# Optimization experiments

Hardware: AMD Instinct MI355X
Metric: run time of the kernel (lower is better)

Reference implementation:

```python
import jax, jax.numpy as jnp
import numpy as np

N_WORDS = 30000
EMB_DIM = 784          # must be a perfect square
MAT_DIM = 28           # sqrt(784)
BATCH = 256
SEQ_LEN = 64


def setup_inputs() -> dict:
    key = jax.random.key(0)
    k_sent, k_w = jax.random.split(key)
    # token ids in [1, N_WORDS]; row 0 of the table is the identity (neutral) element
    sent = jax.random.randint(k_sent, (BATCH, SEQ_LEN), 1, N_WORDS + 1, dtype=jnp.int64) \
        if jax.config.jax_enable_x64 else \
        jax.random.randint(k_sent, (BATCH, SEQ_LEN), 1, N_WORDS + 1, dtype=jnp.int32)
    # 'identity' initialization: N(0, 0.1) + flattened identity, prepended identity neutral row
    eye_flat = jnp.eye(MAT_DIM, dtype=jnp.float32).reshape(-1)        # [784]
    init_w = 0.1 * jax.random.normal(k_w, (N_WORDS, EMB_DIM), dtype=jnp.float32) + eye_flat
    lookup_weight = jnp.concatenate([eye_flat[None, :], init_w], axis=0)  # [N_WORDS+1, 784]
    return {"sent": sent, "lookup_weight": lookup_weight}


def reference(sent, lookup_weight):
    # CMOW: embedding lookup, reshape each word vector to a 28x28 matrix,
    # then a left-to-right chain of matrix products over the sequence.
    B, S = sent.shape
    mats = lookup_weight[sent].reshape(B, S, MAT_DIM, MAT_DIM)   # [B, S, 28, 28]
    # Log-depth parallel prefix product over the sequence axis (matmul is associative).
    prods = jax.lax.associative_scan(lambda a, b: a @ b, mats, axis=1)
    cur_emb = prods[:, -1]                                       # [B, 28, 28]
    return cur_emb.reshape(-1, EMB_DIM)                          # [B, 784]
```

## Files before the change

kernel.cpp:

```cpp
#include <hip/hip_runtime.h>
#include <hip/hip_bf16.h>


typedef float f32x4  __attribute__((ext_vector_type(4)));
typedef float f32x16 __attribute__((ext_vector_type(16)));
typedef short bf16x8 __attribute__((ext_vector_type(8)));

namespace {
constexpr int MD  = 28;
constexpr int EMB = 784;
constexpr int SEQ = 64;
constexpr int BATCH = 256;
constexpr int SEG = 16;
constexpr int LEN = 4;
constexpr int RLP = 33;
}

__device__ __forceinline__ bf16x8 mkfrag(uint32_t w0, uint32_t w1,
                                         uint32_t w2, uint32_t w3) {
  union { uint32_t w[4]; bf16x8 b; } u;
  u.w[0] = w0; u.w[1] = w1; u.w[2] = w2; u.w[3] = w3;
  return u.b;
}

__device__ __forceinline__ void split8(const float* x, bf16x8& hi, bf16x8& lo) {
  uint32_t H[4], L[4];
#pragma unroll
  for (int p = 0; p < 4; ++p) {
    float x0 = x[2 * p], x1 = x[2 * p + 1];
    uint32_t h0 = __float_as_uint(x0) & 0xffff0000u;
    uint32_t h1 = __float_as_uint(x1) & 0xffff0000u;
    float l0 = x0 - __uint_as_float(h0);
    float l1 = x1 - __uint_as_float(h1);
    H[p] = (h0 >> 16) | h1;
    L[p] = (__float_as_uint(l0) >> 16) | (__float_as_uint(l1) & 0xffff0000u);
  }
  hi = mkfrag(H[0], H[1], H[2], H[3]);
  lo = mkfrag(L[0], L[1], L[2], L[3]);
}

__global__ __launch_bounds__(64)
__attribute__((amdgpu_waves_per_eu(3, 4)))
void w2m_partial_mfma(const int* __restrict__ sent,
                      const float* __restrict__ W,
                      float* __restrict__ ws) {
  __shared__ __align__(16) float Ms[1024];
  __shared__ __align__(16) float RL[32 * RLP];

  const int blk   = blockIdx.x;
  const int batch = blk >> 4;
  const int seg   = blk & 15;
  const int lane  = threadIdx.x;
  const int n = lane & 31;
  const int h = lane >> 5;
  const int* srow = sent + batch * SEQ + seg * LEN;

  if (lane < 60) *reinterpret_cast<f32x4*>(&Ms[784 + 4 * lane]) =
      (f32x4){0.f, 0.f, 0.f, 0.f};

  f32x4 st0, st1, st2, st3;
  auto gstage = [&](int t) {
    const f32x4* src = reinterpret_cast<const f32x4*>(W + (size_t)srow[t] * EMB);
    st0 = src[lane];
    st1 = src[64 + lane];
    st2 = src[128 + lane];
    if (lane < 4) st3 = src[192 + lane];
  };
  auto lpublish = [&]() {
    f32x4* d_ = reinterpret_cast<f32x4*>(Ms);
    d_[lane] = st0;
    d_[64 + lane] = st1;
    d_[128 + lane] = st2;
    if (lane < 4) d_[192 + lane] = st3;
  };

  float a[16];
  {
    const float* __restrict__ M0 = W + (size_t)srow[0] * EMB;
    const int m = n;
#pragma unroll
    for (int K = 0; K < 2; ++K)
#pragma unroll
      for (int u = 0; u < 2; ++u) {
        int k0 = 16 * K + 8 * h + 4 * u;
        f32x4 v = {0.f, 0.f, 0.f, 0.f};
        if (m < MD && k0 < MD)
          v = *reinterpret_cast<const f32x4*>(M0 + m * MD + k0);
        a[K * 8 + 4 * u + 0] = v[0];
        a[K * 8 + 4 * u + 1] = v[1];
        a[K * 8 + 4 * u + 2] = v[2];
        a[K * 8 + 4 * u + 3] = v[3];
      }
  }

  gstage(1);
  lpublish();
  gstage(2);

  f32x16 d;
#pragma unroll
  for (int t = 1; t < LEN; ++t) {
    float bb[16];
#pragma unroll
    for (int K = 0; K < 2; ++K)
#pragma unroll
      for (int e = 0; e < 8; ++e) {
        int k = 16 * K + 8 * h + e;
        bb[K * 8 + e] = Ms[k * MD + n];
      }

    bf16x8 ah0, al0, ah1, al1, bh0, bl0, bh1, bl1;
    split8(a,      ah0, al0);
    split8(a + 8,  ah1, al1);
    split8(bb,     bh0, bl0);
    split8(bb + 8, bh1, bl1);

#pragma unroll
    for (int q = 0; q < 16; ++q) d[q] = 0.f;
    d = __builtin_amdgcn_mfma_f32_32x32x16_bf16(ah0, bh0, d, 0, 0, 0);
    d = __builtin_amdgcn_mfma_f32_32x32x16_bf16(ah0, bl0, d, 0, 0, 0);
    d = __builtin_amdgcn_mfma_f32_32x32x16_bf16(al0, bh0, d, 0, 0, 0);
    d = __builtin_amdgcn_mfma_f32_32x32x16_bf16(ah1, bh1, d, 0, 0, 0);
    d = __builtin_amdgcn_mfma_f32_32x32x16_bf16(ah1, bl1, d, 0, 0, 0);
    d = __builtin_amdgcn_mfma_f32_32x32x16_bf16(al1, bh1, d, 0, 0, 0);

    if (t < LEN - 1) {
      lpublish();
      if (t + 2 < LEN) gstage(t + 2);

#pragma unroll
      for (int e = 0; e < 16; ++e) {
        int r = (e & 3) + 8 * (e >> 2) + 4 * h;
        RL[r * RLP + n] = d[e];
      }
      const int m = n;
#pragma unroll
      for (int K = 0; K < 2; ++K)
#pragma unroll
        for (int e = 0; e < 8; ++e) {
          int k = 16 * K + 8 * h + e;
          a[K * 8 + e] = RL[m * RLP + k];
        }
    }
  }

  float* pb = ws + (size_t)(batch * SEG + seg) * EMB;
  if (n < MD) {
    if ((seg & 1) == 0) {
#pragma unroll
      for (int q = 0; q < 4; ++q) {
        int rbase = 8 * q + 4 * h;
        if (rbase < MD) {
          f32x4 v = { d[4 * q], d[4 * q + 1], d[4 * q + 2], d[4 * q + 3] };
          *reinterpret_cast<f32x4*>(pb + n * MD + rbase) = v;
        }
      }
    } else {
#pragma unroll
      for (int e = 0; e < 16; ++e) {
        int r = (e & 3) + 8 * (e >> 2) + 4 * h;
        if (r < MD) pb[r * MD + n] = d[e];
      }
    }
  }
}


__device__ __forceinline__ void kloop(const float* __restrict__ A,
                                      const float* __restrict__ B,
                                      int r0, int c0,
                                      f32x4& a0, f32x4& a1, f32x4& a2, f32x4& a3) {
  f32x4 z = {0.f, 0.f, 0.f, 0.f};
  a0 = a1 = a2 = a3 = z;
#pragma unroll
  for (int k = 0; k < MD; ++k) {
    f32x4 rv = *reinterpret_cast<const f32x4*>(A + k * MD + r0);
    f32x4 mv = *reinterpret_cast<const f32x4*>(B + k * MD + c0);
    a0 += rv[0] * mv;
    a1 += rv[1] * mv;
    a2 += rv[2] * mv;
    a3 += rv[3] * mv;
  }
}

__device__ __forceinline__ void store_T(float* __restrict__ D, int r0, int c0,
                                        const f32x4& a0, const f32x4& a1,
                                        const f32x4& a2, const f32x4& a3) {
#pragma unroll
  for (int cc = 0; cc < 4; ++cc) {
    f32x4 v = { a0[cc], a1[cc], a2[cc], a3[cc] };
    *reinterpret_cast<f32x4*>(D + (c0 + cc) * MD + r0) = v;
  }
}

__device__ __forceinline__ void store_N(float* __restrict__ D, int r0, int c0,
                                        const f32x4& a0, const f32x4& a1,
                                        const f32x4& a2, const f32x4& a3) {
  *reinterpret_cast<f32x4*>(D + (r0 + 0) * MD + c0) = a0;
  *reinterpret_cast<f32x4*>(D + (r0 + 1) * MD + c0) = a1;
  *reinterpret_cast<f32x4*>(D + (r0 + 2) * MD + c0) = a2;
  *reinterpret_cast<f32x4*>(D + (r0 + 3) * MD + c0) = a3;
}

__global__ __launch_bounds__(512, 1)
void w2m_combine(const float* __restrict__ ws, float* __restrict__ out) {
  __shared__ __align__(16) float P[SEG][EMB];
  __shared__ __align__(16) float Q8[8][EMB];
  __shared__ __align__(16) float Q4[4][EMB];
  __shared__ __align__(16) float Q2[2][EMB];

  const int batch = blockIdx.x;
  const int tid   = threadIdx.x;
  const int w     = tid >> 6;
  const int lane  = tid & 63;
  const bool act  = lane < 49;
  const int i = lane / 7, j = lane % 7;
  const int r0 = 4 * i, c0 = 4 * j;

  {
    const f32x4* src = reinterpret_cast<const f32x4*>(ws + (size_t)batch * SEG * EMB);
    f32x4* dst = reinterpret_cast<f32x4*>(&P[0][0]);
    for (int u = tid; u < SEG * EMB / 4; u += 512) dst[u] = src[u];
  }
  __syncthreads();

  f32x4 a0, a1, a2, a3;
  if (act) {
    kloop(P[2 * w], P[2 * w + 1], r0, c0, a0, a1, a2, a3);
    if (w & 1) store_N(Q8[w], r0, c0, a0, a1, a2, a3);
    else       store_T(Q8[w], r0, c0, a0, a1, a2, a3);
  }
  __syncthreads();
  if (w < 4 && act) {
    kloop(Q8[2 * w], Q8[2 * w + 1], r0, c0, a0, a1, a2, a3);
    if (w & 1) store_N(Q4[w], r0, c0, a0, a1, a2, a3);
    else       store_T(Q4[w], r0, c0, a0, a1, a2, a3);
  }
  __syncthreads();
  if (w < 2 && act) {
    kloop(Q4[2 * w], Q4[2 * w + 1], r0, c0, a0, a1, a2, a3);
    if (w & 1) store_N(Q2[w], r0, c0, a0, a1, a2, a3);
    else       store_T(Q2[w], r0, c0, a0, a1, a2, a3);
  }
  __syncthreads();
  if (w == 0 && act) {
    kloop(Q2[0], Q2[1], r0, c0, a0, a1, a2, a3);
    store_N(out + (size_t)batch * EMB, r0, c0, a0, a1, a2, a3);
  }
}

extern "C" void kernel_launch(void* const* d_in, const int* in_sizes, int n_in,
                              void* d_out, int out_size, void* d_ws, size_t ws_size,
                              hipStream_t stream) {
  const int*   sent = (const int*)d_in[0];
  const float* W    = (const float*)d_in[1];
  float*       out  = (float*)d_out;
  float*       ws   = (float*)d_ws;
  (void)in_sizes; (void)n_in; (void)out_size; (void)ws_size;

  w2m_partial_mfma<<<BATCH * SEG, 64, 0, stream>>>(sent, W, ws);
  w2m_combine<<<BATCH, 512, 0, stream>>>(ws, out);
}
```

Baseline: 141.1 us.

## Keep partial chain in registers by computing transposed product with lane shuffles

The partial-product kernel now computes the chain in transposed form. Each new word matrix is loaded straight from global memory into MFMA A-operand registers, and the running product is kept as the B operand. The accumulator layout is turned into the next B fragment with a cross-half __shfl_xor, which removes both shared-memory buffers and the LDS round-trip transpose. Because the result is now transposed, the store orientation for even and odd segments is swapped. In exchange, the kernel does strided uncoalesced global loads per word and more register moves.

```diff
diff --git a/kernel.cpp b/kernel.cpp
--- a/kernel.cpp
+++ b/kernel.cpp
@@ -13,7 +13,6 @@
 constexpr int BATCH = 256;
 constexpr int SEG = 16;
 constexpr int LEN = 4;
-constexpr int RLP = 33;
 }
 
 __device__ __forceinline__ bf16x8 mkfrag(uint32_t w0, uint32_t w1,
@@ -44,76 +43,65 @@
 void w2m_partial_mfma(const int* __restrict__ sent,
                       const float* __restrict__ W,
                       float* __restrict__ ws) {
-  __shared__ __align__(16) float Ms[1024];
-  __shared__ __align__(16) float RL[32 * RLP];
-
   const int blk   = blockIdx.x;
   const int batch = blk >> 4;
   const int seg   = blk & 15;
   const int lane  = threadIdx.x;
-  const int n = lane & 31;
-  const int h = lane >> 5;
+  const int n  = lane & 31;
+  const int h  = lane >> 5;
+  const int nc = n < 27 ? n : 27;
   const int* srow = sent + batch * SEQ + seg * LEN;
 
-  if (lane < 60) *reinterpret_cast<f32x4*>(&Ms[784 + 4 * lane]) =
-      (f32x4){0.f, 0.f, 0.f, 0.f};
-
-  f32x4 st0, st1, st2, st3;
-  auto gstage = [&](int t) {
-    const f32x4* src = reinterpret_cast<const f32x4*>(W + (size_t)srow[t] * EMB);
-    st0 = src[lane];
-    st1 = src[64 + lane];
-    st2 = src[128 + lane];
-    if (lane < 4) st3 = src[192 + lane];
+  auto loadA = [&](int t, float* a) {
+    const float* __restrict__ Mt = W + (size_t)srow[t] * EMB;
+#pragma unroll
+    for (int K = 0; K < 2; ++K)
+#pragma unroll
+      for (int e = 0; e < 8; ++e) {
+        int k = 16 * K + 8 * h + e;
+        float v = 0.f;
+        if (k < MD) v = Mt[k * MD + nc];
+        a[K * 8 + e] = v;
+      }
   };
-  auto lpublish = [&]() {
-    f32x4* d_ = reinterpret_cast<f32x4*>(Ms);
-    d_[lane] = st0;
-    d_[64 + lane] = st1;
-    d_[128 + lane] = st2;
-    if (lane < 4) d_[192 + lane] = st3;
-  };
-
-  float a[16];
+
+  float b0[16];
   {
     const float* __restrict__ M0 = W + (size_t)srow[0] * EMB;
-    const int m = n;
 #pragma unroll
     for (int K = 0; K < 2; ++K)
 #pragma unroll
       for (int u = 0; u < 2; ++u) {
         int k0 = 16 * K + 8 * h + 4 * u;
         f32x4 v = {0.f, 0.f, 0.f, 0.f};
-        if (m < MD && k0 < MD)
-          v = *reinterpret_cast<const f32x4*>(M0 + m * MD + k0);
-        a[K * 8 + 4 * u + 0] = v[0];
-        a[K * 8 + 4 * u + 1] = v[1];
-        a[K * 8 + 4 * u + 2] = v[2];
-        a[K * 8 + 4 * u + 3] = v[3];
-      }
-  }
-
-  gstage(1);
-  lpublish();
-  gstage(2);
+        if (k0 < MD)
+          v = *reinterpret_cast<const f32x4*>(M0 + nc * MD + k0);
+        b0[K * 8 + 4 * u + 0] = v[0];
+        b0[K * 8 + 4 * u + 1] = v[1];
+        b0[K * 8 + 4 * u + 2] = v[2];
+        b0[K * 8 + 4 * u + 3] = v[3];
+      }
+  }
+
+  float a_cur[16], a_nxt[16];
+  loadA(1, a_cur);
+  loadA(2, a_nxt);
+
+  bf16x8 bh0, bl0, bh1, bl1;
+  split8(b0,     bh0, bl0);
+  split8(b0 + 8, bh1, bl1);
 
   f32x16 d;
 #pragma unroll
   for (int t = 1; t < LEN; ++t) {
-    float bb[16];
-#pragma unroll
-    for (int K = 0; K < 2; ++K)
-#pragma unroll
-      for (int e = 0; e < 8; ++e) {
-        int k = 16 * K + 8 * h + e;
-        bb[K * 8 + e] = Ms[k * MD + n];
-      }
-
-    bf16x8 ah0, al0, ah1, al1, bh0, bl0, bh1, bl1;
-    split8(a,      ah0, al0);
-    split8(a + 8,  ah1, al1);
-    split8(bb,     bh0, bl0);
-    split8(bb + 8, bh1, bl1);
+    bf16x8 ah0, al0, ah1, al1;
+    split8(a_cur,     ah0, al0);
+    split8(a_cur + 8, ah1, al1);
+    if (t + 1 < LEN) {
+#pragma unroll
+      for (int q = 0; q < 16; ++q) a_cur[q] = a_nxt[q];
+      if (t + 2 < LEN) loadA(t + 2, a_nxt);
+    }
 
 #pragma unroll
     for (int q = 0; q < 16; ++q) d[q] = 0.f;
@@ -125,22 +113,19 @@
     d = __builtin_amdgcn_mfma_f32_32x32x16_bf16(al1, bh1, d, 0, 0, 0);
 
     if (t < LEN - 1) {
-      lpublish();
-      if (t + 2 < LEN) gstage(t + 2);
-
-#pragma unroll
-      for (int e = 0; e < 16; ++e) {
-        int r = (e & 3) + 8 * (e >> 2) + 4 * h;
-        RL[r * RLP + n] = d[e];
-      }
-      const int m = n;
+      float s_[16];
+#pragma unroll
+      for (int e = 0; e < 16; ++e) s_[e] = __shfl_xor((float)d[e], 32);
+      float bb[16];
 #pragma unroll
       for (int K = 0; K < 2; ++K)
 #pragma unroll
-        for (int e = 0; e < 8; ++e) {
-          int k = 16 * K + 8 * h + e;
-          a[K * 8 + e] = RL[m * RLP + k];
+        for (int e = 0; e < 4; ++e) {
+          bb[K * 8 + e]     = h ? s_[e + 4 + 8 * K] : (float)d[e + 8 * K];
+          bb[K * 8 + e + 4] = h ? (float)d[e + 4 + 8 * K] : s_[e + 8 * K];
         }
+      split8(bb,     bh0, bl0);
+      split8(bb + 8, bh1, bl1);
     }
   }
 
@@ -148,18 +133,18 @@
   if (n < MD) {
     if ((seg & 1) == 0) {
 #pragma unroll
-      for (int q = 0; q < 4; ++q) {
-        int rbase = 8 * q + 4 * h;
-        if (rbase < MD) {
-          f32x4 v = { d[4 * q], d[4 * q + 1], d[4 * q + 2], d[4 * q + 3] };
-          *reinterpret_cast<f32x4*>(pb + n * MD + rbase) = v;
-        }
-      }
-    } else {
-#pragma unroll
       for (int e = 0; e < 16; ++e) {
         int r = (e & 3) + 8 * (e >> 2) + 4 * h;
         if (r < MD) pb[r * MD + n] = d[e];
+      }
+    } else {
+#pragma unroll
+      for (int q = 0; q < 4; ++q) {
+        int r0 = 8 * q + 4 * h;
+        if (r0 < MD) {
+          f32x4 v = { d[4 * q], d[4 * q + 1], d[4 * q + 2], d[4 * q + 3] };
+          *reinterpret_cast<f32x4*>(pb + n * MD + r0) = v;
+        }
       }
     }
   }
```

Result: no change. 142.5 us (+1.0%).
